# Kernel tuning notes

Hardware: AMD Instinct MI355X
Metric: run time of the kernel (lower is better)

## Reference

```python
import jax, jax.numpy as jnp
import numpy as np

N1 = 50000
N2 = 50000
E = 800000
D = 128
DOUT = 128
L = 2
NEG_SLOPE = 0.2


def setup_inputs() -> dict:
    key = jax.random.key(0)
    ks = jax.random.split(key, 32)
    s = 0.05
    inp = {
        "x1": jax.random.normal(ks[0], (N1, D), jnp.float32),
        "x2": jax.random.normal(ks[1], (N2, D), jnp.float32),
        "ei11": jax.random.randint(ks[2], (2, E), 0, N1, jnp.int32),
        "ei22": jax.random.randint(ks[3], (2, E), 0, N2, jnp.int32),
        "ei12": jnp.stack([
            jax.random.randint(ks[4], (E,), 0, N1, jnp.int32),
            jax.random.randint(ks[5], (E,), 0, N2, jnp.int32),
        ]),
        # intra protein_1 GATConv params (shared lin for src/dst), stacked over layers
        "W_i1": jax.random.normal(ks[6], (L, D, D), jnp.float32) * s,
        "as_i1": jax.random.normal(ks[7], (L, D), jnp.float32) * s,
        "ad_i1": jax.random.normal(ks[8], (L, D), jnp.float32) * s,
        "b_i1": jnp.zeros((L, D), jnp.float32),
        # intra protein_2
        "W_i2": jax.random.normal(ks[9], (L, D, D), jnp.float32) * s,
        "as_i2": jax.random.normal(ks[10], (L, D), jnp.float32) * s,
        "ad_i2": jax.random.normal(ks[11], (L, D), jnp.float32) * s,
        "b_i2": jnp.zeros((L, D), jnp.float32),
        # inter protein_1 -> protein_2 (bipartite: separate src/dst lin)
        "Ws_x": jax.random.normal(ks[12], (L, D, D), jnp.float32) * s,
        "Wd_x": jax.random.normal(ks[13], (L, D, D), jnp.float32) * s,
        "as_x": jax.random.normal(ks[14], (L, D), jnp.float32) * s,
        "ad_x": jax.random.normal(ks[15], (L, D), jnp.float32) * s,
        "b_x": jnp.zeros((L, D), jnp.float32),
        # final linear
        "W_out": jax.random.normal(ks[16], (D, DOUT), jnp.float32) * s,
        "b_out": jnp.zeros((DOUT,), jnp.float32),
    }
    return inp


def _segment_softmax(logits, seg, num_segments):
    m = jax.ops.segment_max(logits, seg, num_segments=num_segments)
    e = jnp.exp(logits - m[seg])
    z = jax.ops.segment_sum(e, seg, num_segments=num_segments)
    return e / (z[seg] + 1e-16)


def _gat(x_src, x_dst, ei, W_src, W_dst, a_s, a_d, b, num_dst):
    hs = x_src @ W_src                       # [Ns, D]
    hd = x_dst @ W_dst                       # [Nd, D]
    src, dst = ei[0], ei[1]
    logit = jax.nn.leaky_relu((hs @ a_s)[src] + (hd @ a_d)[dst], NEG_SLOPE)  # [E]
    coef = _segment_softmax(logit, dst, num_dst)  # [E]
    out = jax.ops.segment_sum(coef[:, None] * hs[src], dst, num_segments=num_dst)
    return out + b


def reference(x1, x2, ei11, ei22, ei12, W_i1, as_i1, ad_i1, b_i1,
              W_i2, as_i2, ad_i2, b_i2, Ws_x, Wd_x, as_x, ad_x, b_x,
              W_out, b_out):
    h1, h2 = x1, x2
    for l in range(L):
        o1 = _gat(h1, h1, ei11, W_i1[l], W_i1[l], as_i1[l], ad_i1[l], b_i1[l], N1)
        o2 = _gat(h2, h2, ei22, W_i2[l], W_i2[l], as_i2[l], ad_i2[l], b_i2[l], N2)
        o2 = o2 + _gat(h1, h2, ei12, Ws_x[l], Wd_x[l], as_x[l], ad_x[l], b_x[l], N2)
        h1 = jax.nn.relu(o1)
        h2 = jax.nn.relu(o2)
    return (h1 @ W_out + b_out, h2 @ W_out + b_out)
```

## Files before the change

### kernel.cpp

```cpp
#include <hip/hip_runtime.h>
#include <hip/hip_bf16.h>
#include <hip/hip_fp16.h>
#include <cstdint>

#define D 128
#define NEG 0.2f
#define WSH 8
#define WIN 256
#define CAP 5120

typedef _Float16 f16x8 __attribute__((ext_vector_type(8)));
typedef float f32x4 __attribute__((ext_vector_type(4)));

static __device__ __forceinline__ ushort f2h(float x) {
  __half h = __float2half(x);
  return *reinterpret_cast<ushort*>(&h);
}
static __device__ __forceinline__ float h2f(ushort u) {
  __half h = *reinterpret_cast<__half*>(&u);
  return __half2float(h);
}

__global__ __launch_bounds__(256) void bin3_kernel(
    const int* __restrict__ ei0, const int* __restrict__ ei1, const int* __restrict__ ei2,
    int E0, int E1, int E2,
    int* __restrict__ p0, int* __restrict__ p1, int* __restrict__ p2,
    int* __restrict__ bcnt) {
  int sset = blockIdx.y;
  const int* ei = sset == 0 ? ei0 : (sset == 1 ? ei1 : ei2);
  int E = sset == 0 ? E0 : (sset == 1 ? E1 : E2);
  int* pairs = sset == 0 ? p0 : (sset == 1 ? p1 : p2);
  int* bc = bcnt + sset * 256;
  const int* src = ei;
  const int* dst = ei + E;
  __shared__ int lcnt[WIN], lcur[WIN], lbase[WIN];
  int t = threadIdx.x;
  lcnt[t] = 0; lcur[t] = 0;
  __syncthreads();
  int base = blockIdx.x * 2048;
  int s[8], d[8];
  #pragma unroll
  for (int k = 0; k < 8; k++) {
    int e = base + k * 256 + t;
    if (e < E) {
      s[k] = src[e]; d[k] = dst[e];
      atomicAdd(&lcnt[d[k] >> WSH], 1);
    } else d[k] = -1;
  }
  __syncthreads();
  if (lcnt[t] > 0) lbase[t] = atomicAdd(&bc[t], lcnt[t]);
  __syncthreads();
  #pragma unroll
  for (int k = 0; k < 8; k++) {
    if (d[k] >= 0) {
      int b = d[k] >> WSH;
      int r = atomicAdd(&lcur[b], 1);
      int slot = lbase[b] + r;
      if (slot < CAP)
        pairs[(size_t)b * CAP + slot] = (s[k] & 0xFFFF) | ((d[k] & 255) << 16);
    }
  }
}

__global__ __launch_bounds__(256) void count3_kernel(
    const int* __restrict__ p0, const int* __restrict__ p1, const int* __restrict__ p2,
    const int* __restrict__ bcnt,
    int* __restrict__ cnt0, int* __restrict__ cnt1, int* __restrict__ cnt2,
    int* __restrict__ off0, int* __restrict__ off1, int* __restrict__ off2,
    int* __restrict__ wsum, int N0, int N1, int N2) {
  int sset = blockIdx.y;
  const int* pairs = sset == 0 ? p0 : (sset == 1 ? p1 : p2);
  int* cnt = sset == 0 ? cnt0 : (sset == 1 ? cnt1 : cnt2);
  int* offs = sset == 0 ? off0 : (sset == 1 ? off1 : off2);
  int N = sset == 0 ? N0 : (sset == 1 ? N1 : N2);
  const int* bc = bcnt + sset * 256;
  int* ws = wsum + sset * 256;
  __shared__ int h[WIN];
  __shared__ int sc[WIN];
  int b = blockIdx.x, t = threadIdx.x;
  h[t] = 0; __syncthreads();
  int n = bc[b]; if (n > CAP) n = CAP;
  const int* p = pairs + (size_t)b * CAP;
  for (int i = t; i < n; i += 256) atomicAdd(&h[(p[i] >> 16) & 255], 1);
  __syncthreads();
  int v = h[t]; sc[t] = v; __syncthreads();
  for (int o = 1; o < 256; o <<= 1) {
    int x = (t >= o) ? sc[t - o] : 0; __syncthreads();
    sc[t] += x; __syncthreads();
  }
  int node = b * WIN + t;
  if (node < N) { cnt[node] = v; offs[node] = sc[t] - v; }
  if (t == 255) ws[b] = sc[255];
}

__global__ void wscan3_kernel(int* wsum) {
  __shared__ int sc[256];
  int t = threadIdx.x;
  int* w = wsum + blockIdx.x * 256;
  int v = w[t];
  sc[t] = v; __syncthreads();
  for (int o = 1; o < 256; o <<= 1) {
    int x = (t >= o) ? sc[t - o] : 0; __syncthreads();
    sc[t] += x; __syncthreads();
  }
  w[t] = sc[t] - v;
}

__global__ __launch_bounds__(256) void fill23_kernel(
    const int* __restrict__ p0, const int* __restrict__ p1, const int* __restrict__ p2,
    const int* __restrict__ bcnt, const int* __restrict__ wsum,
    int* __restrict__ off0, int* __restrict__ off1, int* __restrict__ off2,
    ushort* __restrict__ cs0, ushort* __restrict__ cs1, ushort* __restrict__ cs2,
    int N0, int N1, int N2) {
  int sset = blockIdx.y;
  const int* pairs = sset == 0 ? p0 : (sset == 1 ? p1 : p2);
  int* offs = sset == 0 ? off0 : (sset == 1 ? off1 : off2);
  ushort* csrc = sset == 0 ? cs0 : (sset == 1 ? cs1 : cs2);
  int N = sset == 0 ? N0 : (sset == 1 ? N1 : N2);
  const int* bc = bcnt + sset * 256;
  __shared__ int cur[WIN];
  int b = blockIdx.x, t = threadIdx.x;
  int wb = wsum[sset * 256 + b];
  int node = b * WIN + t;
  int start = 0;
  if (node < N) { start = offs[node] + wb; offs[node] = start; }
  cur[t] = start;
  __syncthreads();
  int n = bc[b]; if (n > CAP) n = CAP;
  const int* p = pairs + (size_t)b * CAP;
  for (int i = t; i < n; i += 256) {
    int v = p[i];
    int pp = atomicAdd(&cur[(v >> 16) & 255], 1);
    csrc[pp] = (ushort)(v & 0xFFFF);
  }
}

__global__ __launch_bounds__(256) void wprep6_kernel(
    const float* __restrict__ W_i1, const float* __restrict__ W_i2,
    const float* __restrict__ Ws_x,
    ushort* __restrict__ WtA, ushort* __restrict__ WtB, ushort* __restrict__ WtX) {
  int b = blockIdx.x;
  int which = b >> 1, l = b & 1;
  const float* Wb = (which == 0 ? W_i1 : (which == 1 ? W_i2 : Ws_x)) + l * 16384;
  ushort* Wo = (which == 0 ? WtA : (which == 1 ? WtB : WtX)) + l * 16384;
  __shared__ float s[128 * 129];
  int t = threadIdx.x;
  #pragma unroll
  for (int i = 0; i < 16; i++) {
    int idx = i * 256 + t;
    int k = idx >> 5, n4 = idx & 31;
    float4 v = *(const float4*)&Wb[k * 128 + n4 * 4];
    s[k * 129 + n4 * 4 + 0] = v.x;
    s[k * 129 + n4 * 4 + 1] = v.y;
    s[k * 129 + n4 * 4 + 2] = v.z;
    s[k * 129 + n4 * 4 + 3] = v.w;
  }
  __syncthreads();
  #pragma unroll
  for (int i = 0; i < 8; i++) {
    int idx = i * 256 + t;
    int n = idx >> 4, k8 = (idx & 15) * 8;
    ushort4 h0, h1;
    h0.x = f2h(s[(k8 + 0) * 129 + n]); h0.y = f2h(s[(k8 + 1) * 129 + n]);
    h0.z = f2h(s[(k8 + 2) * 129 + n]); h0.w = f2h(s[(k8 + 3) * 129 + n]);
    h1.x = f2h(s[(k8 + 4) * 129 + n]); h1.y = f2h(s[(k8 + 5) * 129 + n]);
    h1.z = f2h(s[(k8 + 6) * 129 + n]); h1.w = f2h(s[(k8 + 7) * 129 + n]);
    *(ushort4*)&Wo[n * 128 + k8] = h0;
    *(ushort4*)&Wo[n * 128 + k8 + 4] = h1;
  }
}

__global__ __launch_bounds__(256) void wprepout_kernel(
    const float* __restrict__ W, ushort* __restrict__ Wh, ushort* __restrict__ Wl) {
  __shared__ float s[128 * 129];
  int t = threadIdx.x;
  #pragma unroll
  for (int i = 0; i < 16; i++) {
    int idx = i * 256 + t;
    int k = idx >> 5, n4 = idx & 31;
    float4 v = *(const float4*)&W[k * 128 + n4 * 4];
    s[k * 129 + n4 * 4 + 0] = v.x;
    s[k * 129 + n4 * 4 + 1] = v.y;
    s[k * 129 + n4 * 4 + 2] = v.z;
    s[k * 129 + n4 * 4 + 3] = v.w;
  }
  __syncthreads();
  #pragma unroll
  for (int i = 0; i < 8; i++) {
    int idx = i * 256 + t;
    int n = idx >> 4, k8 = (idx & 15) * 8;
    ushort hh[8], ll[8];
    #pragma unroll
    for (int e = 0; e < 8; e++) {
      float w = s[(k8 + e) * 129 + n];
      hh[e] = f2h(w);
      ll[e] = f2h(w - h2f(hh[e]));
    }
    *(ushort4*)&Wh[n * 128 + k8]     = make_ushort4(hh[0], hh[1], hh[2], hh[3]);
    *(ushort4*)&Wh[n * 128 + k8 + 4] = make_ushort4(hh[4], hh[5], hh[6], hh[7]);
    *(ushort4*)&Wl[n * 128 + k8]     = make_ushort4(ll[0], ll[1], ll[2], ll[3]);
    *(ushort4*)&Wl[n * 128 + k8 + 4] = make_ushort4(ll[4], ll[5], ll[6], ll[7]);
  }
}

__global__ void wvec2_kernel(const float* __restrict__ Wd, const float* __restrict__ ad,
                             float* __restrict__ wv) {
  int l = blockIdx.x;
  int r = threadIdx.x;
  const float* Wb = Wd + (size_t)l * 16384;
  const float* ab = ad + l * 128;
  float s = 0.f;
  for (int c = 0; c < D; c++) s += Wb[r * D + c] * ab[c];
  wv[l * 128 + r] = s;
}

#define SWZ(b) ((b) ^ ((((b) >> 8) & 7) << 4))

template <int XF16>
__global__ __launch_bounds__(256) void gemm16_kernel(
    const void* __restrict__ Xv, const ushort* __restrict__ Wt,
    ushort* __restrict__ Yb,
    const float* __restrict__ a_sv, const float* __restrict__ a_dv,
    const float* __restrict__ wvec,
    float* __restrict__ aSo, float* __restrict__ aDo, float* __restrict__ aXo, int M) {
  __shared__ ushort sX[64 * 128];
  __shared__ ushort sW[128 * 128];
  __shared__ float sv[128];
  int t = threadIdx.x;
  int bm = blockIdx.x * 64;
  {
    const uint4* W4 = (const uint4*)Wt;
    #pragma unroll
    for (int i = 0; i < 8; i++) {
      int idx = i * 256 + t;
      int byte = idx * 16;
      *(uint4*)((char*)sW + SWZ(byte)) = W4[idx];
    }
  }
  {
    #pragma unroll
    for (int i = 0; i < 8; i++) {
      int idx = i * 256 + t;
      int row = idx >> 5, c4 = idx & 31;
      ushort4 h = make_ushort4(0, 0, 0, 0);
      if (bm + row < M) {
        if (XF16) {
          h = *(const ushort4*)((const ushort*)Xv + (size_t)(bm + row) * 128 + c4 * 4);
        } else {
          float4 v = ((const float4*)Xv)[(size_t)(bm + row) * 32 + c4];
          h.x = f2h(v.x); h.y = f2h(v.y); h.z = f2h(v.z); h.w = f2h(v.w);
        }
      }
      int byte = idx * 8;
      *(uint2*)((char*)sX + SWZ(byte)) = *(uint2*)&h;
    }
  }
  if (wvec != nullptr && t < 128) sv[t] = wvec[t];
  __syncthreads();

  int w = t >> 6, l = t & 63;
  int lq = l >> 4, lr = l & 15;
  int xrow = w * 16 + lr;
  f32x4 acc[8] = {};
  float ax = 0.f;
  #pragma unroll
  for (int kk = 0; kk < 4; kk++) {
    int xb = xrow * 256 + kk * 64 + lq * 16;
    f16x8 xa = *(const f16x8*)((const char*)sX + SWZ(xb));
    if (wvec != nullptr) {
      float4 w0 = *(const float4*)&sv[kk * 32 + lq * 8];
      float4 w1 = *(const float4*)&sv[kk * 32 + lq * 8 + 4];
      ax += (float)xa[0] * w0.x + (float)xa[1] * w0.y + (float)xa[2] * w0.z + (float)xa[3] * w0.w
          + (float)xa[4] * w1.x + (float)xa[5] * w1.y + (float)xa[6] * w1.z + (float)xa[7] * w1.w;
    }
    #pragma unroll
    for (int ct = 0; ct < 8; ct++) {
      int nb = (ct * 16 + lr) * 256 + kk * 64 + lq * 16;
      f16x8 wa = *(const f16x8*)((const char*)sW + SWZ(nb));
      acc[ct] = __builtin_amdgcn_mfma_f32_16x16x32_f16(wa, xa, acc[ct], 0, 0, 0);
    }
  }
  int row_m = bm + xrow;
  bool valid = row_m < M;
  #pragma unroll
  for (int ct = 0; ct < 8; ct++) {
    ushort4 h;
    h.x = f2h(acc[ct][0]); h.y = f2h(acc[ct][1]);
    h.z = f2h(acc[ct][2]); h.w = f2h(acc[ct][3]);
    if (valid) *(ushort4*)&Yb[(size_t)row_m * 128 + ct * 16 + lq * 4] = h;
  }
  if (a_sv != nullptr) {
    float s = 0.f;
    #pragma unroll
    for (int ct = 0; ct < 8; ct++) {
      float4 a = *(const float4*)&a_sv[ct * 16 + lq * 4];
      s += acc[ct][0] * a.x + acc[ct][1] * a.y + acc[ct][2] * a.z + acc[ct][3] * a.w;
    }
    s += __shfl_xor(s, 16); s += __shfl_xor(s, 32);
    if (valid && lq == 0) aSo[row_m] = s;
  }
  if (a_dv != nullptr) {
    float s = 0.f;
    #pragma unroll
    for (int ct = 0; ct < 8; ct++) {
      float4 a = *(const float4*)&a_dv[ct * 16 + lq * 4];
      s += acc[ct][0] * a.x + acc[ct][1] * a.y + acc[ct][2] * a.z + acc[ct][3] * a.w;
    }
    s += __shfl_xor(s, 16); s += __shfl_xor(s, 32);
    if (valid && lq == 0) aDo[row_m] = s;
  }
  if (wvec != nullptr) {
    ax += __shfl_xor(ax, 16); ax += __shfl_xor(ax, 32);
    if (valid && lq == 0) aXo[row_m] = ax;
  }
}

template <int XF16>
__global__ __launch_bounds__(256) void gemmx2_kernel(
    const void* __restrict__ Xv,
    const ushort* __restrict__ Wt0, const ushort* __restrict__ Wt1,
    ushort* __restrict__ Yb0, ushort* __restrict__ Yb1,
    const float* __restrict__ asv0, const float* __restrict__ asv1,
    const float* __restrict__ adv1,
    float* __restrict__ aSo0, float* __restrict__ aSo1, float* __restrict__ aDo1,
    int M) {
  int y = blockIdx.y;
  const ushort* Wt = y ? Wt1 : Wt0;
  ushort* Yb = y ? Yb1 : Yb0;
  const float* a_sv = y ? asv1 : asv0;
  const float* a_dv = y ? adv1 : nullptr;
  float* aSo = y ? aSo1 : aSo0;
  float* aDo = aDo1;
  __shared__ ushort sX[64 * 128];
  __shared__ ushort sW[128 * 128];
  int t = threadIdx.x;
  int bm = blockIdx.x * 64;
  {
    const uint4* W4 = (const uint4*)Wt;
    #pragma unroll
    for (int i = 0; i < 8; i++) {
      int idx = i * 256 + t;
      int byte = idx * 16;
      *(uint4*)((char*)sW + SWZ(byte)) = W4[idx];
    }
  }
  {
    #pragma unroll
    for (int i = 0; i < 8; i++) {
      int idx = i * 256 + t;
      int row = idx >> 5, c4 = idx & 31;
      ushort4 h = make_ushort4(0, 0, 0, 0);
      if (bm + row < M) {
        if (XF16) {
          h = *(const ushort4*)((const ushort*)Xv + (size_t)(bm + row) * 128 + c4 * 4);
        } else {
          float4 v = ((const float4*)Xv)[(size_t)(bm + row) * 32 + c4];
          h.x = f2h(v.x); h.y = f2h(v.y); h.z = f2h(v.z); h.w = f2h(v.w);
        }
      }
      int byte = idx * 8;
      *(uint2*)((char*)sX + SWZ(byte)) = *(uint2*)&h;
    }
  }
  __syncthreads();
  int w = t >> 6, l = t & 63;
  int lq = l >> 4, lr = l & 15;
  int xrow = w * 16 + lr;
  f32x4 acc[8] = {};
  #pragma unroll
  for (int kk = 0; kk < 4; kk++) {
    int xb = xrow * 256 + kk * 64 + lq * 16;
    f16x8 xa = *(const f16x8*)((const char*)sX + SWZ(xb));
    #pragma unroll
    for (int ct = 0; ct < 8; ct++) {
      int nb = (ct * 16 + lr) * 256 + kk * 64 + lq * 16;
      f16x8 wa = *(const f16x8*)((const char*)sW + SWZ(nb));
      acc[ct] = __builtin_amdgcn_mfma_f32_16x16x32_f16(wa, xa, acc[ct], 0, 0, 0);
    }
  }
  int row_m = bm + xrow;
  bool valid = row_m < M;
  #pragma unroll
  for (int ct = 0; ct < 8; ct++) {
    ushort4 h;
    h.x = f2h(acc[ct][0]); h.y = f2h(acc[ct][1]);
    h.z = f2h(acc[ct][2]); h.w = f2h(acc[ct][3]);
    if (valid) *(ushort4*)&Yb[(size_t)row_m * 128 + ct * 16 + lq * 4] = h;
  }
  {
    float s = 0.f;
    #pragma unroll
    for (int ct = 0; ct < 8; ct++) {
      float4 a = *(const float4*)&a_sv[ct * 16 + lq * 4];
      s += acc[ct][0] * a.x + acc[ct][1] * a.y + acc[ct][2] * a.z + acc[ct][3] * a.w;
    }
    s += __shfl_xor(s, 16); s += __shfl_xor(s, 32);
    if (valid && lq == 0) aSo[row_m] = s;
  }
  if (a_dv != nullptr) {
    float s = 0.f;
    #pragma unroll
    for (int ct = 0; ct < 8; ct++) {
      float4 a = *(const float4*)&a_dv[ct * 16 + lq * 4];
      s += acc[ct][0] * a.x + acc[ct][1] * a.y + acc[ct][2] * a.z + acc[ct][3] * a.w;
    }
    s += __shfl_xor(s, 16); s += __shfl_xor(s, 32);
    if (valid && lq == 0) aDo[row_m] = s;
  }
}

__global__ __launch_bounds__(512) void gemmfin_kernel(
    const ushort* __restrict__ XA, const ushort* __restrict__ XB,
    const ushort* __restrict__ Wh, const ushort* __restrict__ Wl,
    const float* __restrict__ bias,
    float* __restrict__ YA, float* __restrict__ YB, int MA, int MB, int mgA) {
  int bid = blockIdx.x;
  const ushort* X; float* Y; int M, bm;
  if (bid < mgA) { X = XA; Y = YA; M = MA; bm = bid * 128; }
  else           { X = XB; Y = YB; M = MB; bm = (bid - mgA) * 128; }
  __shared__ ushort sWh[128 * 128];
  __shared__ ushort sWl[128 * 128];
  __shared__ ushort sH[128 * 128];
  int t = threadIdx.x;
  {
    const uint4* Wh4 = (const uint4*)Wh;
    const uint4* Wl4 = (const uint4*)Wl;
    #pragma unroll
    for (int i = 0; i < 4; i++) {
      int idx = i * 512 + t;
      int byte = idx * 16;
      *(uint4*)((char*)sWh + SWZ(byte)) = Wh4[idx];
      *(uint4*)((char*)sWl + SWZ(byte)) = Wl4[idx];
    }
  }
  {
    const uint4* X4 = (const uint4*)X;
    #pragma unroll
    for (int i = 0; i < 4; i++) {
      int idx = i * 512 + t;
      int row = idx >> 4, c8 = idx & 15;
      uint4 v = make_uint4(0, 0, 0, 0);
      if (bm + row < M) v = X4[(size_t)(bm + row) * 16 + c8];
      *(uint4*)((char*)sH + SWZ(idx * 16)) = v;
    }
  }
  __syncthreads();
  int w = t >> 6, l = t & 63;
  int lq = l >> 4, lr = l & 15;
  int xrow = w * 16 + lr;
  f32x4 acc[8] = {};
  #pragma unroll
  for (int kk = 0; kk < 4; kk++) {
    int xb = xrow * 256 + kk * 64 + lq * 16;
    f16x8 xh = *(const f16x8*)((const char*)sH + SWZ(xb));
    #pragma unroll
    for (int ct = 0; ct < 8; ct++) {
      int nb = (ct * 16 + lr) * 256 + kk * 64 + lq * 16;
      f16x8 wh = *(const f16x8*)((const char*)sWh + SWZ(nb));
      f16x8 wl = *(const f16x8*)((const char*)sWl + SWZ(nb));
      acc[ct] = __builtin_amdgcn_mfma_f32_16x16x32_f16(wh, xh, acc[ct], 0, 0, 0);
      acc[ct] = __builtin_amdgcn_mfma_f32_16x16x32_f16(wl, xh, acc[ct], 0, 0, 0);
    }
  }
  int row_m = bm + xrow;
  if (row_m < M) {
    #pragma unroll
    for (int ct = 0; ct < 8; ct++) {
      float4 b = *(const float4*)&bias[ct * 16 + lq * 4];
      float4 o = make_float4(acc[ct][0] + b.x, acc[ct][1] + b.y,
                             acc[ct][2] + b.z, acc[ct][3] + b.w);
      *(float4*)&Y[(size_t)row_m * 128 + ct * 16 + lq * 4] = o;
    }
  }
}

static __device__ __forceinline__ void gather_rows(
    const ushort* __restrict__ hs, const float* __restrict__ aSv, float adv,
    int st, int deg, const ushort* __restrict__ cs,
    int lane, int quarter, int q, float acc[8], float& z) {
  for (int base = 0; base < deg; base += 64) {
    int m = deg - base; if (m > 64) m = 64;
    int sidx = 0; float el = 0.f;
    if (lane < m) {
      sidx = cs[st + base + lane];
      float l = aSv[sidx] + adv;
      l = (l > 0.f) ? l : NEG * l;
      el = __expf(l);
    }
    float zs = el;
    for (int o = 32; o > 0; o >>= 1) zs += __shfl_xor(zs, o);
    z += zs;
    #pragma unroll 4
    for (int j = 0; j < m; j += 4) {
      int jj = j + quarter;
      int sj = __shfl(sidx, jj);
      float ej = __shfl(el, jj);
      uint4 hv = *(const uint4*)(hs + (size_t)sj * D + q * 8);
      float2 f0 = __half22float2(*reinterpret_cast<__half2*>(&hv.x));
      float2 f1 = __half22float2(*reinterpret_cast<__half2*>(&hv.y));
      float2 f2 = __half22float2(*reinterpret_cast<__half2*>(&hv.z));
      float2 f3 = __half22float2(*reinterpret_cast<__half2*>(&hv.w));
      acc[0] += ej * f0.x; acc[1] += ej * f0.y;
      acc[2] += ej * f1.x; acc[3] += ej * f1.y;
      acc[4] += ej * f2.x; acc[5] += ej * f2.y;
      acc[6] += ej * f3.x; acc[7] += ej * f3.y;
    }
  }
}

__global__ __launch_bounds__(256) void agg1_kernel(
    const ushort* __restrict__ hs, const float* __restrict__ aS, const float* __restrict__ aD,
    const int* __restrict__ offs, const int* __restrict__ cnt, const ushort* __restrict__ csrc,
    const float* __restrict__ bias1, ushort* __restrict__ out, int N) {
  int wid = threadIdx.x >> 6, lane = threadIdx.x & 63;
  int d = blockIdx.x * 4 + wid;
  if (d >= N) return;
  int quarter = lane >> 4, q = lane & 15;
  float acc[8] = {}; float z = 0.f;
  gather_rows(hs, aS, aD[d], offs[d], cnt[d], csrc, lane, quarter, q, acc, z);
  float inv = 1.f / (z + 1e-16f);
  float res[8];
  #pragma unroll
  for (int k = 0; k < 8; k++) res[k] = acc[k] * inv;
  #pragma unroll
  for (int k = 0; k < 8; k++) {
    res[k] += __shfl_xor(res[k], 16);
    res[k] += __shfl_xor(res[k], 32);
  }
  if (quarter == 0) {
    float4 b0 = *(const float4*)(bias1 + q * 8);
    float4 b1 = *(const float4*)(bias1 + q * 8 + 4);
    res[0]+=b0.x; res[1]+=b0.y; res[2]+=b0.z; res[3]+=b0.w;
    res[4]+=b1.x; res[5]+=b1.y; res[6]+=b1.z; res[7]+=b1.w;
    #pragma unroll
    for (int k = 0; k < 8; k++) res[k] = res[k] > 0.f ? res[k] : 0.f;
    size_t rb = (size_t)d * D + q * 8;
    *(ushort4*)(out + rb)     = make_ushort4(f2h(res[0]), f2h(res[1]), f2h(res[2]), f2h(res[3]));
    *(ushort4*)(out + rb + 4) = make_ushort4(f2h(res[4]), f2h(res[5]), f2h(res[6]), f2h(res[7]));
  }
}

__global__ __launch_bounds__(256) void agg2_kernel(
    const ushort* __restrict__ hs1, const float* __restrict__ aS1, const float* __restrict__ aD1,
    const int* __restrict__ off1, const int* __restrict__ cnt1, const ushort* __restrict__ cs1,
    const ushort* __restrict__ hs2, const float* __restrict__ aS2v, const float* __restrict__ aD2v,
    const int* __restrict__ off2, const int* __restrict__ cnt2, const ushort* __restrict__ cs2,
    const float* __restrict__ bias1, const float* __restrict__ bias2,
    ushort* __restrict__ out, int N) {
  int wid = threadIdx.x >> 6, lane = threadIdx.x & 63;
  int d = blockIdx.x * 4 + wid;
  if (d >= N) return;
  int quarter = lane >> 4, q = lane & 15;
  float acc1[8] = {}; float z1 = 0.f;
  gather_rows(hs1, aS1, aD1[d], off1[d], cnt1[d], cs1, lane, quarter, q, acc1, z1);
  float acc2[8] = {}; float z2 = 0.f;
  gather_rows(hs2, aS2v, aD2v[d], off2[d], cnt2[d], cs2, lane, quarter, q, acc2, z2);
  float inv1 = 1.f / (z1 + 1e-16f);
  float inv2 = 1.f / (z2 + 1e-16f);
  float res[8];
  #pragma unroll
  for (int k = 0; k < 8; k++) res[k] = acc1[k] * inv1 + acc2[k] * inv2;
  #pragma unroll
  for (int k = 0; k < 8; k++) {
    res[k] += __shfl_xor(res[k], 16);
    res[k] += __shfl_xor(res[k], 32);
  }
  if (quarter == 0) {
    float4 b0 = *(const float4*)(bias1 + q * 8);
    float4 b1 = *(const float4*)(bias1 + q * 8 + 4);
    float4 c0 = *(const float4*)(bias2 + q * 8);
    float4 c1 = *(const float4*)(bias2 + q * 8 + 4);
    res[0]+=b0.x+c0.x; res[1]+=b0.y+c0.y; res[2]+=b0.z+c0.z; res[3]+=b0.w+c0.w;
    res[4]+=b1.x+c1.x; res[5]+=b1.y+c1.y; res[6]+=b1.z+c1.z; res[7]+=b1.w+c1.w;
    #pragma unroll
    for (int k = 0; k < 8; k++) res[k] = res[k] > 0.f ? res[k] : 0.f;
    size_t rb = (size_t)d * D + q * 8;
    *(ushort4*)(out + rb)     = make_ushort4(f2h(res[0]), f2h(res[1]), f2h(res[2]), f2h(res[3]));
    *(ushort4*)(out + rb + 4) = make_ushort4(f2h(res[4]), f2h(res[5]), f2h(res[6]), f2h(res[7]));
  }
}

extern "C" void kernel_launch(void* const* d_in, const int* in_sizes, int n_in,
                              void* d_out, int out_size, void* d_ws, size_t ws_size,
                              hipStream_t stream) {
  const float* x1   = (const float*)d_in[0];
  const float* x2   = (const float*)d_in[1];
  const int*   ei11 = (const int*)d_in[2];
  const int*   ei22 = (const int*)d_in[3];
  const int*   ei12 = (const int*)d_in[4];
  const float* W_i1 = (const float*)d_in[5];
  const float* as_i1= (const float*)d_in[6];
  const float* ad_i1= (const float*)d_in[7];
  const float* b_i1 = (const float*)d_in[8];
  const float* W_i2 = (const float*)d_in[9];
  const float* as_i2= (const float*)d_in[10];
  const float* ad_i2= (const float*)d_in[11];
  const float* b_i2 = (const float*)d_in[12];
  const float* Ws_x = (const float*)d_in[13];
  const float* Wd_x = (const float*)d_in[14];
  const float* as_x = (const float*)d_in[15];
  const float* ad_x = (const float*)d_in[16];
  const float* b_x  = (const float*)d_in[17];
  const float* W_out= (const float*)d_in[18];
  const float* b_out= (const float*)d_in[19];

  int N1 = in_sizes[0] / D, N2 = in_sizes[1] / D;
  int E11 = in_sizes[2] / 2, E22 = in_sizes[3] / 2, E12 = in_sizes[4] / 2;
  int Nmax = (N1 > N2) ? N1 : N2;
  int Emax = E11 > E22 ? (E11 > E12 ? E11 : E12) : (E22 > E12 ? E22 : E12);
  int NB1 = (N1 + WIN - 1) / WIN, NB2 = (N2 + WIN - 1) / WIN;
  int NBmax = (NB1 > NB2) ? NB1 : NB2;

  float* outA = (float*)d_out;
  float* outB = outA + (size_t)N1 * D;

  char* w = (char*)d_ws;
  auto alloc = [&](size_t b) { char* p = w; w += (b + 255) & ~(size_t)255; return p; };
  size_t pair_bytes = (size_t)NBmax * CAP * 4;
  size_t hsmax = (size_t)Nmax * D * 2;
  ushort* BB  = (ushort*)alloc(hsmax > pair_bytes ? hsmax : pair_bytes);
  ushort* BX  = (ushort*)alloc(hsmax > pair_bytes ? hsmax : pair_bytes);
  ushort* h1  = (ushort*)alloc(((size_t)N1 * D * 2) > pair_bytes ? ((size_t)N1 * D * 2) : pair_bytes);
  ushort* h2  = (ushort*)alloc((size_t)N2 * D * 2);
  int* pairs0 = (int*)BB;
  int* pairs1 = (int*)BX;
  int* pairs2 = (int*)h1;
  float* aS   = (float*)alloc((size_t)Nmax * 4);
  float* aD   = (float*)alloc((size_t)Nmax * 4);
  float* aDx  = (float*)alloc((size_t)Nmax * 4);
  float* aS2  = (float*)alloc((size_t)Nmax * 4);
  float* wvecB= (float*)alloc(256 * 4);
  ushort* WtA = (ushort*)alloc(2 * 16384 * 2);
  ushort* WtB = (ushort*)alloc(2 * 16384 * 2);
  ushort* WtX = (ushort*)alloc(2 * 16384 * 2);
  ushort* Wfh = (ushort*)alloc(16384 * 2);
  ushort* Wfl = (ushort*)alloc(16384 * 2);
  int* bcnt  = (int*)alloc(3 * 256 * 4);
  int* wsum  = (int*)alloc(3 * 256 * 4);
  int* cnt11 = (int*)alloc((size_t)N1 * 4);
  int* off11 = (int*)alloc((size_t)N1 * 4);
  ushort* csA = (ushort*)alloc((size_t)E11 * 2);
  int* cnt22 = (int*)alloc((size_t)N2 * 4);
  int* off22 = (int*)alloc((size_t)N2 * 4);
  ushort* csB = (ushort*)alloc((size_t)E22 * 2);
  int* cnt12 = (int*)alloc((size_t)N2 * 4);
  int* off12 = (int*)alloc((size_t)N2 * 4);
  ushort* csC = (ushort*)alloc((size_t)E12 * 2);

  hipMemsetAsync(bcnt, 0, 3 * 256 * 4, stream);
  bin3_kernel<<<dim3((Emax + 2047) / 2048, 3), 256, 0, stream>>>(
      ei11, ei22, ei12, E11, E22, E12, pairs0, pairs1, pairs2, bcnt);
  count3_kernel<<<dim3(NBmax, 3), 256, 0, stream>>>(
      pairs0, pairs1, pairs2, bcnt, cnt11, cnt22, cnt12,
      off11, off22, off12, wsum, N1, N2, N2);
  wscan3_kernel<<<3, 256, 0, stream>>>(wsum);
  fill23_kernel<<<dim3(NBmax, 3), 256, 0, stream>>>(
      pairs0, pairs1, pairs2, bcnt, wsum, off11, off22, off12,
      csA, csB, csC, N1, N2, N2);

  wprep6_kernel<<<6, 256, 0, stream>>>(W_i1, W_i2, Ws_x, WtA, WtB, WtX);
  wprepout_kernel<<<1, 256, 0, stream>>>(W_out, Wfh, Wfl);
  wvec2_kernel<<<2, 128, 0, stream>>>(Wd_x, ad_x, wvecB);

  int mg1 = (N1 + 63) / 64, mg2 = (N2 + 63) / 64;
  int fg1 = (N1 + 127) / 128, fg2 = (N2 + 127) / 128;
  int gg1 = (N1 + 3) / 4, gg2 = (N2 + 3) / 4;
  ushort* hsA = BB;
  ushort* hsB = BB;
  ushort* hsX = BX;

  gemmx2_kernel<0><<<dim3(mg1, 2), 256, 0, stream>>>(x1, WtX, WtA, hsX, hsA,
      as_x, as_i1, ad_i1, aS2, aS, aD, N1);
  agg1_kernel<<<gg1, 256, 0, stream>>>(hsA, aS, aD, off11, cnt11, csA, b_i1, h1, N1);
  gemm16_kernel<0><<<mg2, 256, 0, stream>>>(x2, WtB, hsB,
      as_i2, ad_i2, wvecB, aS, aD, aDx, N2);
  agg2_kernel<<<gg2, 256, 0, stream>>>(hsB, aS, aD, off22, cnt22, csB,
      hsX, aS2, aDx, off12, cnt12, csC, b_i2, b_x, h2, N2);

  gemmx2_kernel<1><<<dim3(mg1, 2), 256, 0, stream>>>(h1, WtX + 16384, WtA + 16384,
      hsX, hsA, as_x + 128, as_i1 + 128, ad_i1 + 128, aS2, aS, aD, N1);
  agg1_kernel<<<gg1, 256, 0, stream>>>(hsA, aS, aD, off11, cnt11, csA,
      b_i1 + 128, h1, N1);
  gemm16_kernel<1><<<mg2, 256, 0, stream>>>(h2, WtB + 16384, hsB,
      as_i2 + 128, ad_i2 + 128, wvecB + 128, aS, aD, aDx, N2);
  agg2_kernel<<<gg2, 256, 0, stream>>>(hsB, aS, aD, off22, cnt22, csB,
      hsX, aS2, aDx, off12, cnt12, csC, b_i2 + 128, b_x + 128, h2, N2);

  gemmfin_kernel<<<fg1 + fg2, 512, 0, stream>>>(h1, h2, Wfh, Wfl, b_out,
                                                outA, outB, N1, N2, fg1);
}
```

Before: 384.0 us.

## Fuse CSR build, weight prep, and per-layer GEMMs into fewer launches

Merges the count, window-scan and fill stages of CSR construction into one kernel, with each block redoing the small 256-entry prefix scan over bin counts. Folds the three weight-prep kernels into one launch. Fuses the three per-layer projection GEMMs (inter, intra-1, intra-2) into a single 3-way grid by giving each GEMM its own output buffers, removing launch overhead and a serialization point. Also unrolls the gather loop by four so independent row loads are in flight together, at the cost of extra buffers and registers.

```diff
diff --git a/kernel.cpp b/kernel.cpp
--- a/kernel.cpp
+++ b/kernel.cpp
@@ -62,89 +62,78 @@
   }
 }
 
-__global__ __launch_bounds__(256) void count3_kernel(
+__global__ __launch_bounds__(256) void countfill3_kernel(
     const int* __restrict__ p0, const int* __restrict__ p1, const int* __restrict__ p2,
     const int* __restrict__ bcnt,
     int* __restrict__ cnt0, int* __restrict__ cnt1, int* __restrict__ cnt2,
-    int* __restrict__ off0, int* __restrict__ off1, int* __restrict__ off2,
-    int* __restrict__ wsum, int N0, int N1, int N2) {
-  int sset = blockIdx.y;
-  const int* pairs = sset == 0 ? p0 : (sset == 1 ? p1 : p2);
-  int* cnt = sset == 0 ? cnt0 : (sset == 1 ? cnt1 : cnt2);
-  int* offs = sset == 0 ? off0 : (sset == 1 ? off1 : off2);
-  int N = sset == 0 ? N0 : (sset == 1 ? N1 : N2);
-  const int* bc = bcnt + sset * 256;
-  int* ws = wsum + sset * 256;
-  __shared__ int h[WIN];
-  __shared__ int sc[WIN];
-  int b = blockIdx.x, t = threadIdx.x;
-  h[t] = 0; __syncthreads();
-  int n = bc[b]; if (n > CAP) n = CAP;
-  const int* p = pairs + (size_t)b * CAP;
-  for (int i = t; i < n; i += 256) atomicAdd(&h[(p[i] >> 16) & 255], 1);
-  __syncthreads();
-  int v = h[t]; sc[t] = v; __syncthreads();
-  for (int o = 1; o < 256; o <<= 1) {
-    int x = (t >= o) ? sc[t - o] : 0; __syncthreads();
-    sc[t] += x; __syncthreads();
-  }
-  int node = b * WIN + t;
-  if (node < N) { cnt[node] = v; offs[node] = sc[t] - v; }
-  if (t == 255) ws[b] = sc[255];
-}
-
-__global__ void wscan3_kernel(int* wsum) {
-  __shared__ int sc[256];
-  int t = threadIdx.x;
-  int* w = wsum + blockIdx.x * 256;
-  int v = w[t];
-  sc[t] = v; __syncthreads();
-  for (int o = 1; o < 256; o <<= 1) {
-    int x = (t >= o) ? sc[t - o] : 0; __syncthreads();
-    sc[t] += x; __syncthreads();
-  }
-  w[t] = sc[t] - v;
-}
-
-__global__ __launch_bounds__(256) void fill23_kernel(
-    const int* __restrict__ p0, const int* __restrict__ p1, const int* __restrict__ p2,
-    const int* __restrict__ bcnt, const int* __restrict__ wsum,
     int* __restrict__ off0, int* __restrict__ off1, int* __restrict__ off2,
     ushort* __restrict__ cs0, ushort* __restrict__ cs1, ushort* __restrict__ cs2,
     int N0, int N1, int N2) {
   int sset = blockIdx.y;
   const int* pairs = sset == 0 ? p0 : (sset == 1 ? p1 : p2);
+  int* cnt = sset == 0 ? cnt0 : (sset == 1 ? cnt1 : cnt2);
   int* offs = sset == 0 ? off0 : (sset == 1 ? off1 : off2);
   ushort* csrc = sset == 0 ? cs0 : (sset == 1 ? cs1 : cs2);
   int N = sset == 0 ? N0 : (sset == 1 ? N1 : N2);
   const int* bc = bcnt + sset * 256;
-  __shared__ int cur[WIN];
+  __shared__ int h[WIN], sc[WIN], wbs[WIN], cur[WIN];
   int b = blockIdx.x, t = threadIdx.x;
-  int wb = wsum[sset * 256 + b];
+  int bcv = bc[t]; if (bcv > CAP) bcv = CAP;
+  wbs[t] = bcv;
+  h[t] = 0;
+  __syncthreads();
+  for (int o = 1; o < 256; o <<= 1) {
+    int x = (t >= o) ? wbs[t - o] : 0; __syncthreads();
+    wbs[t] += x; __syncthreads();
+  }
+  int n = bc[b]; if (n > CAP) n = CAP;
+  int wb = wbs[b] - n;
+  const int* p = pairs + (size_t)b * CAP;
+  for (int i = t; i < n; i += 256) atomicAdd(&h[(p[i] >> 16) & 255], 1);
+  __syncthreads();
+  int v = h[t]; sc[t] = v;
+  __syncthreads();
+  for (int o = 1; o < 256; o <<= 1) {
+    int x = (t >= o) ? sc[t - o] : 0; __syncthreads();
+    sc[t] += x; __syncthreads();
+  }
+  int start = sc[t] - v + wb;
   int node = b * WIN + t;
-  int start = 0;
-  if (node < N) { start = offs[node] + wb; offs[node] = start; }
+  if (node < N) { cnt[node] = v; offs[node] = start; }
   cur[t] = start;
   __syncthreads();
-  int n = bc[b]; if (n > CAP) n = CAP;
-  const int* p = pairs + (size_t)b * CAP;
   for (int i = t; i < n; i += 256) {
-    int v = p[i];
-    int pp = atomicAdd(&cur[(v >> 16) & 255], 1);
-    csrc[pp] = (ushort)(v & 0xFFFF);
-  }
-}
-
-__global__ __launch_bounds__(256) void wprep6_kernel(
+    int pv = p[i];
+    int pp = atomicAdd(&cur[(pv >> 16) & 255], 1);
+    csrc[pp] = (ushort)(pv & 0xFFFF);
+  }
+}
+
+__global__ __launch_bounds__(256) void prep_kernel(
     const float* __restrict__ W_i1, const float* __restrict__ W_i2,
-    const float* __restrict__ Ws_x,
-    ushort* __restrict__ WtA, ushort* __restrict__ WtB, ushort* __restrict__ WtX) {
+    const float* __restrict__ Ws_x, const float* __restrict__ W_out,
+    const float* __restrict__ Wd_x, const float* __restrict__ ad_x,
+    ushort* __restrict__ WtA, ushort* __restrict__ WtB, ushort* __restrict__ WtX,
+    ushort* __restrict__ Wfh, ushort* __restrict__ Wfl, float* __restrict__ wv) {
   int b = blockIdx.x;
-  int which = b >> 1, l = b & 1;
-  const float* Wb = (which == 0 ? W_i1 : (which == 1 ? W_i2 : Ws_x)) + l * 16384;
-  ushort* Wo = (which == 0 ? WtA : (which == 1 ? WtB : WtX)) + l * 16384;
+  int t = threadIdx.x;
+  if (b >= 7) {
+    int l = b - 7;
+    if (t < 128) {
+      const float* Wb = Wd_x + (size_t)l * 16384;
+      const float* ab = ad_x + l * 128;
+      float s = 0.f;
+      for (int c = 0; c < D; c++) s += Wb[t * D + c] * ab[c];
+      wv[l * 128 + t] = s;
+    }
+    return;
+  }
   __shared__ float s[128 * 129];
-  int t = threadIdx.x;
+  const float* Wb;
+  if (b < 6) {
+    int which = b >> 1, l = b & 1;
+    Wb = (which == 0 ? W_i1 : (which == 1 ? W_i2 : Ws_x)) + l * 16384;
+  } else Wb = W_out;
   #pragma unroll
   for (int i = 0; i < 16; i++) {
     int idx = i * 256 + t;
@@ -156,85 +145,77 @@
     s[k * 129 + n4 * 4 + 3] = v.w;
   }
   __syncthreads();
-  #pragma unroll
-  for (int i = 0; i < 8; i++) {
-    int idx = i * 256 + t;
-    int n = idx >> 4, k8 = (idx & 15) * 8;
-    ushort4 h0, h1;
-    h0.x = f2h(s[(k8 + 0) * 129 + n]); h0.y = f2h(s[(k8 + 1) * 129 + n]);
-    h0.z = f2h(s[(k8 + 2) * 129 + n]); h0.w = f2h(s[(k8 + 3) * 129 + n]);
-    h1.x = f2h(s[(k8 + 4) * 129 + n]); h1.y = f2h(s[(k8 + 5) * 129 + n]);
-    h1.z = f2h(s[(k8 + 6) * 129 + n]); h1.w = f2h(s[(k8 + 7) * 129 + n]);
-    *(ushort4*)&Wo[n * 128 + k8] = h0;
-    *(ushort4*)&Wo[n * 128 + k8 + 4] = h1;
-  }
-}
-
-__global__ __launch_bounds__(256) void wprepout_kernel(
-    const float* __restrict__ W, ushort* __restrict__ Wh, ushort* __restrict__ Wl) {
-  __shared__ float s[128 * 129];
-  int t = threadIdx.x;
-  #pragma unroll
-  for (int i = 0; i < 16; i++) {
-    int idx = i * 256 + t;
-    int k = idx >> 5, n4 = idx & 31;
-    float4 v = *(const float4*)&W[k * 128 + n4 * 4];
-    s[k * 129 + n4 * 4 + 0] = v.x;
-    s[k * 129 + n4 * 4 + 1] = v.y;
-    s[k * 129 + n4 * 4 + 2] = v.z;
-    s[k * 129 + n4 * 4 + 3] = v.w;
-  }
-  __syncthreads();
-  #pragma unroll
-  for (int i = 0; i < 8; i++) {
-    int idx = i * 256 + t;
-    int n = idx >> 4, k8 = (idx & 15) * 8;
-    ushort hh[8], ll[8];
-    #pragma unroll
-    for (int e = 0; e < 8; e++) {
-      float w = s[(k8 + e) * 129 + n];
-      hh[e] = f2h(w);
-      ll[e] = f2h(w - h2f(hh[e]));
-    }
-    *(ushort4*)&Wh[n * 128 + k8]     = make_ushort4(hh[0], hh[1], hh[2], hh[3]);
-    *(ushort4*)&Wh[n * 128 + k8 + 4] = make_ushort4(hh[4], hh[5], hh[6], hh[7]);
-    *(ushort4*)&Wl[n * 128 + k8]     = make_ushort4(ll[0], ll[1], ll[2], ll[3]);
-    *(ushort4*)&Wl[n * 128 + k8 + 4] = make_ushort4(ll[4], ll[5], ll[6], ll[7]);
-  }
-}
-
-__global__ void wvec2_kernel(const float* __restrict__ Wd, const float* __restrict__ ad,
-                             float* __restrict__ wv) {
-  int l = blockIdx.x;
-  int r = threadIdx.x;
-  const float* Wb = Wd + (size_t)l * 16384;
-  const float* ab = ad + l * 128;
-  float s = 0.f;
-  for (int c = 0; c < D; c++) s += Wb[r * D + c] * ab[c];
-  wv[l * 128 + r] = s;
+  if (b < 6) {
+    int which = b >> 1, l = b & 1;
+    ushort* Wo = (which == 0 ? WtA : (which == 1 ? WtB : WtX)) + l * 16384;
+    #pragma unroll
+    for (int i = 0; i < 8; i++) {
+      int idx = i * 256 + t;
+      int n = idx >> 4, k8 = (idx & 15) * 8;
+      ushort4 h0, h1;
+      h0.x = f2h(s[(k8 + 0) * 129 + n]); h0.y = f2h(s[(k8 + 1) * 129 + n]);
+      h0.z = f2h(s[(k8 + 2) * 129 + n]); h0.w = f2h(s[(k8 + 3) * 129 + n]);
+      h1.x = f2h(s[(k8 + 4) * 129 + n]); h1.y = f2h(s[(k8 + 5) * 129 + n]);
+      h1.z = f2h(s[(k8 + 6) * 129 + n]); h1.w = f2h(s[(k8 + 7) * 129 + n]);
+      *(ushort4*)&Wo[n * 128 + k8] = h0;
+      *(ushort4*)&Wo[n * 128 + k8 + 4] = h1;
+    }
+  } else {
+    #pragma unroll
+    for (int i = 0; i < 8; i++) {
+      int idx = i * 256 + t;
+      int n = idx >> 4, k8 = (idx & 15) * 8;
+      ushort hh[8], ll[8];
+      #pragma unroll
+      for (int e = 0; e < 8; e++) {
+        float w = s[(k8 + e) * 129 + n];
+        hh[e] = f2h(w);
+        ll[e] = f2h(w - h2f(hh[e]));
+      }
+      *(ushort4*)&Wfh[n * 128 + k8]     = make_ushort4(hh[0], hh[1], hh[2], hh[3]);
+      *(ushort4*)&Wfh[n * 128 + k8 + 4] = make_ushort4(hh[4], hh[5], hh[6], hh[7]);
+      *(ushort4*)&Wfl[n * 128 + k8]     = make_ushort4(ll[0], ll[1], ll[2], ll[3]);
+      *(ushort4*)&Wfl[n * 128 + k8 + 4] = make_ushort4(ll[4], ll[5], ll[6], ll[7]);
+    }
+  }
 }
 
 #define SWZ(b) ((b) ^ ((((b) >> 8) & 7) << 4))
 
 template <int XF16>
-__global__ __launch_bounds__(256) void gemm16_kernel(
-    const void* __restrict__ Xv, const ushort* __restrict__ Wt,
-    ushort* __restrict__ Yb,
-    const float* __restrict__ a_sv, const float* __restrict__ a_dv,
-    const float* __restrict__ wvec,
-    float* __restrict__ aSo, float* __restrict__ aDo, float* __restrict__ aXo, int M) {
+__global__ __launch_bounds__(256) void gemmx3_kernel(
+    const void* __restrict__ Xv1, const void* __restrict__ Xv2,
+    const ushort* __restrict__ WtX_, const ushort* __restrict__ WtA_,
+    const ushort* __restrict__ WtB_,
+    ushort* __restrict__ YbX, ushort* __restrict__ YbA, ushort* __restrict__ YbB,
+    const float* __restrict__ asx, const float* __restrict__ as1,
+    const float* __restrict__ ad1, const float* __restrict__ as2,
+    const float* __restrict__ ad2, const float* __restrict__ wvec,
+    float* __restrict__ aSxo, float* __restrict__ aS1o, float* __restrict__ aD1o,
+    float* __restrict__ aS2o, float* __restrict__ aD2o, float* __restrict__ aXo,
+    int M1, int M2) {
+  int y = blockIdx.y;
+  const void* Xv = (y == 2) ? Xv2 : Xv1;
+  int M = (y == 2) ? M2 : M1;
+  int bm = blockIdx.x * 64;
+  if (bm >= M) return;
+  const ushort* Wt = y == 0 ? WtX_ : (y == 1 ? WtA_ : WtB_);
+  ushort* Yb = y == 0 ? YbX : (y == 1 ? YbA : YbB);
+  const float* a_sv = y == 0 ? asx : (y == 1 ? as1 : as2);
+  const float* a_dv = y == 0 ? nullptr : (y == 1 ? ad1 : ad2);
+  const float* wv = (y == 2) ? wvec : nullptr;
+  float* aSo = y == 0 ? aSxo : (y == 1 ? aS1o : aS2o);
+  float* aDo = (y == 1) ? aD1o : aD2o;
   __shared__ ushort sX[64 * 128];
   __shared__ ushort sW[128 * 128];
   __shared__ float sv[128];
   int t = threadIdx.x;
-  int bm = blockIdx.x * 64;
   {
     const uint4* W4 = (const uint4*)Wt;
     #pragma unroll
     for (int i = 0; i < 8; i++) {
       int idx = i * 256 + t;
-      int byte = idx * 16;
-      *(uint4*)((char*)sW + SWZ(byte)) = W4[idx];
+      *(uint4*)((char*)sW + SWZ(idx * 16)) = W4[idx];
     }
   }
   {
@@ -251,11 +232,10 @@
           h.x = f2h(v.x); h.y = f2h(v.y); h.z = f2h(v.z); h.w = f2h(v.w);
         }
       }
-      int byte = idx * 8;
-      *(uint2*)((char*)sX + SWZ(byte)) = *(uint2*)&h;
-    }
-  }
-  if (wvec != nullptr && t < 128) sv[t] = wvec[t];
+      *(uint2*)((char*)sX + SWZ(idx * 8)) = *(uint2*)&h;
+    }
+  }
+  if (wv != nullptr && t < 128) sv[t] = wv[t];
   __syncthreads();
 
   int w = t >> 6, l = t & 63;
@@ -267,7 +247,7 @@
   for (int kk = 0; kk < 4; kk++) {
     int xb = xrow * 256 + kk * 64 + lq * 16;
     f16x8 xa = *(const f16x8*)((const char*)sX + SWZ(xb));
-    if (wvec != nullptr) {
+    if (wv != nullptr) {
       float4 w0 = *(const float4*)&sv[kk * 32 + lq * 8];
       float4 w1 = *(const float4*)&sv[kk * 32 + lq * 8 + 4];
       ax += (float)xa[0] * w0.x + (float)xa[1] * w0.y + (float)xa[2] * w0.z + (float)xa[3] * w0.w
@@ -289,7 +269,7 @@
     h.z = f2h(acc[ct][2]); h.w = f2h(acc[ct][3]);
     if (valid) *(ushort4*)&Yb[(size_t)row_m * 128 + ct * 16 + lq * 4] = h;
   }
-  if (a_sv != nullptr) {
+  {
     float s = 0.f;
     #pragma unroll
     for (int ct = 0; ct < 8; ct++) {
@@ -309,103 +289,9 @@
     s += __shfl_xor(s, 16); s += __shfl_xor(s, 32);
     if (valid && lq == 0) aDo[row_m] = s;
   }
-  if (wvec != nullptr) {
+  if (wv != nullptr) {
     ax += __shfl_xor(ax, 16); ax += __shfl_xor(ax, 32);
     if (valid && lq == 0) aXo[row_m] = ax;
-  }
-}
-
-template <int XF16>
-__global__ __launch_bounds__(256) void gemmx2_kernel(
-    const void* __restrict__ Xv,
-    const ushort* __restrict__ Wt0, const ushort* __restrict__ Wt1,
-    ushort* __restrict__ Yb0, ushort* __restrict__ Yb1,
-    const float* __restrict__ asv0, const float* __restrict__ asv1,
-    const float* __restrict__ adv1,
-    float* __restrict__ aSo0, float* __restrict__ aSo1, float* __restrict__ aDo1,
-    int M) {
-  int y = blockIdx.y;
-  const ushort* Wt = y ? Wt1 : Wt0;
-  ushort* Yb = y ? Yb1 : Yb0;
-  const float* a_sv = y ? asv1 : asv0;
-  const float* a_dv = y ? adv1 : nullptr;
-  float* aSo = y ? aSo1 : aSo0;
-  float* aDo = aDo1;
-  __shared__ ushort sX[64 * 128];
-  __shared__ ushort sW[128 * 128];
-  int t = threadIdx.x;
-  int bm = blockIdx.x * 64;
-  {
-    const uint4* W4 = (const uint4*)Wt;
-    #pragma unroll
-    for (int i = 0; i < 8; i++) {
-      int idx = i * 256 + t;
-      int byte = idx * 16;
-      *(uint4*)((char*)sW + SWZ(byte)) = W4[idx];
-    }
-  }
-  {
-    #pragma unroll
-    for (int i = 0; i < 8; i++) {
-      int idx = i * 256 + t;
-      int row = idx >> 5, c4 = idx & 31;
-      ushort4 h = make_ushort4(0, 0, 0, 0);
-      if (bm + row < M) {
-        if (XF16) {
-          h = *(const ushort4*)((const ushort*)Xv + (size_t)(bm + row) * 128 + c4 * 4);
-        } else {
-          float4 v = ((const float4*)Xv)[(size_t)(bm + row) * 32 + c4];
-          h.x = f2h(v.x); h.y = f2h(v.y); h.z = f2h(v.z); h.w = f2h(v.w);
-        }
-      }
-      int byte = idx * 8;
-      *(uint2*)((char*)sX + SWZ(byte)) = *(uint2*)&h;
-    }
-  }
-  __syncthreads();
-  int w = t >> 6, l = t & 63;
-  int lq = l >> 4, lr = l & 15;
-  int xrow = w * 16 + lr;
-  f32x4 acc[8] = {};
-  #pragma unroll
-  for (int kk = 0; kk < 4; kk++) {
-    int xb = xrow * 256 + kk * 64 + lq * 16;
-    f16x8 xa = *(const f16x8*)((const char*)sX + SWZ(xb));
-    #pragma unroll
-    for (int ct = 0; ct < 8; ct++) {
-      int nb = (ct * 16 + lr) * 256 + kk * 64 + lq * 16;
-      f16x8 wa = *(const f16x8*)((const char*)sW + SWZ(nb));
-      acc[ct] = __builtin_amdgcn_mfma_f32_16x16x32_f16(wa, xa, acc[ct], 0, 0, 0);
-    }
-  }
-  int row_m = bm + xrow;
-  bool valid = row_m < M;
-  #pragma unroll
-  for (int ct = 0; ct < 8; ct++) {
-    ushort4 h;
-    h.x = f2h(acc[ct][0]); h.y = f2h(acc[ct][1]);
-    h.z = f2h(acc[ct][2]); h.w = f2h(acc[ct][3]);
-    if (valid) *(ushort4*)&Yb[(size_t)row_m * 128 + ct * 16 + lq * 4] = h;
-  }
-  {
-    float s = 0.f;
-    #pragma unroll
-    for (int ct = 0; ct < 8; ct++) {
-      float4 a = *(const float4*)&a_sv[ct * 16 + lq * 4];
-      s += acc[ct][0] * a.x + acc[ct][1] * a.y + acc[ct][2] * a.z + acc[ct][3] * a.w;
-    }
-    s += __shfl_xor(s, 16); s += __shfl_xor(s, 32);
-    if (valid && lq == 0) aSo[row_m] = s;
-  }
-  if (a_dv != nullptr) {
-    float s = 0.f;
-    #pragma unroll
-    for (int ct = 0; ct < 8; ct++) {
-      float4 a = *(const float4*)&a_dv[ct * 16 + lq * 4];
-      s += acc[ct][0] * a.x + acc[ct][1] * a.y + acc[ct][2] * a.z + acc[ct][3] * a.w;
-    }
-    s += __shfl_xor(s, 16); s += __shfl_xor(s, 32);
-    if (valid && lq == 0) aDo[row_m] = s;
   }
 }
 
@@ -428,9 +314,8 @@
     #pragma unroll
     for (int i = 0; i < 4; i++) {
       int idx = i * 512 + t;
-      int byte = idx * 16;
-      *(uint4*)((char*)sWh + SWZ(byte)) = Wh4[idx];
-      *(uint4*)((char*)sWl + SWZ(byte)) = Wl4[idx];
+      *(uint4*)((char*)sWh + SWZ(idx * 16)) = Wh4[idx];
+      *(uint4*)((char*)sWl + SWZ(idx * 16)) = Wl4[idx];
     }
   }
   {
@@ -473,6 +358,16 @@
     }
   }
 }
+
+#define ACC8(hv, ej) { \
+  float2 f0 = __half22float2(*reinterpret_cast<__half2*>(&hv.x)); \
+  float2 f1 = __half22float2(*reinterpret_cast<__half2*>(&hv.y)); \
+  float2 f2 = __half22float2(*reinterpret_cast<__half2*>(&hv.z)); \
+  float2 f3 = __half22float2(*reinterpret_cast<__half2*>(&hv.w)); \
+  acc[0] += ej * f0.x; acc[1] += ej * f0.y; \
+  acc[2] += ej * f1.x; acc[3] += ej * f1.y; \
+  acc[4] += ej * f2.x; acc[5] += ej * f2.y; \
+  acc[6] += ej * f3.x; acc[7] += ej * f3.y; }
 
 static __device__ __forceinline__ void gather_rows(
     const ushort* __restrict__ hs, const float* __restrict__ aSv, float adv,
@@ -490,20 +385,20 @@
     float zs = el;
     for (int o = 32; o > 0; o >>= 1) zs += __shfl_xor(zs, o);
     z += zs;
-    #pragma unroll 4
-    for (int j = 0; j < m; j += 4) {
-      int jj = j + quarter;
-      int sj = __shfl(sidx, jj);
-      float ej = __shfl(el, jj);
-      uint4 hv = *(const uint4*)(hs + (size_t)sj * D + q * 8);
-      float2 f0 = __half22float2(*reinterpret_cast<__half2*>(&hv.x));
-      float2 f1 = __half22float2(*reinterpret_cast<__half2*>(&hv.y));
-      float2 f2 = __half22float2(*reinterpret_cast<__half2*>(&hv.z));
-      float2 f3 = __half22float2(*reinterpret_cast<__half2*>(&hv.w));
-      acc[0] += ej * f0.x; acc[1] += ej * f0.y;
-      acc[2] += ej * f1.x; acc[3] += ej * f1.y;
-      acc[4] += ej * f2.x; acc[5] += ej * f2.y;
-      acc[6] += ej * f3.x; acc[7] += ej * f3.y;
+    for (int j = 0; j < m; j += 16) {
+      int s0 = __shfl(sidx, j + quarter);
+      int s1 = __shfl(sidx, j + 4 + quarter);
+      int s2 = __shfl(sidx, j + 8 + quarter);
+      int s3 = __shfl(sidx, j + 12 + quarter);
+      float e0 = __shfl(el, j + quarter);
+      float e1 = __shfl(el, j + 4 + quarter);
+      float e2 = __shfl(el, j + 8 + quarter);
+      float e3 = __shfl(el, j + 12 + quarter);
+      uint4 h0 = *(const uint4*)(hs + (size_t)s0 * D + q * 8);
+      uint4 h1 = *(const uint4*)(hs + (size_t)s1 * D + q * 8);
+      uint4 h2 = *(const uint4*)(hs + (size_t)s2 * D + q * 8);
+      uint4 h3 = *(const uint4*)(hs + (size_t)s3 * D + q * 8);
+      ACC8(h0, e0); ACC8(h1, e1); ACC8(h2, e2); ACC8(h3, e3);
     }
   }
 }
@@ -552,9 +447,15 @@
   if (d >= N) return;
   int quarter = lane >> 4, q = lane & 15;
   float acc1[8] = {}; float z1 = 0.f;
-  gather_rows(hs1, aS1, aD1[d], off1[d], cnt1[d], cs1, lane, quarter, q, acc1, z1);
+  {
+    float* acc = acc1;
+    gather_rows(hs1, aS1, aD1[d], off1[d], cnt1[d], cs1, lane, quarter, q, acc, z1);
+  }
   float acc2[8] = {}; float z2 = 0.f;
-  gather_rows(hs2, aS2v, aD2v[d], off2[d], cnt2[d], cs2, lane, quarter, q, acc2, z2);
+  {
+    float* acc = acc2;
+    gather_rows(hs2, aS2v, aD2v[d], off2[d], cnt2[d], cs2, lane, quarter, q, acc, z2);
+  }
   float inv1 = 1.f / (z1 + 1e-16f);
   float inv2 = 1.f / (z2 + 1e-16f);
   float res[8];
@@ -618,17 +519,21 @@
   auto alloc = [&](size_t b) { char* p = w; w += (b + 255) & ~(size_t)255; return p; };
   size_t pair_bytes = (size_t)NBmax * CAP * 4;
   size_t hsmax = (size_t)Nmax * D * 2;
-  ushort* BB  = (ushort*)alloc(hsmax > pair_bytes ? hsmax : pair_bytes);
-  ushort* BX  = (ushort*)alloc(hsmax > pair_bytes ? hsmax : pair_bytes);
-  ushort* h1  = (ushort*)alloc(((size_t)N1 * D * 2) > pair_bytes ? ((size_t)N1 * D * 2) : pair_bytes);
+  size_t big = hsmax > pair_bytes ? hsmax : pair_bytes;
+  ushort* BA  = (ushort*)alloc(big);
+  ushort* BX  = (ushort*)alloc(big);
+  ushort* h1  = (ushort*)alloc(big);
+  ushort* BB2 = (ushort*)alloc(hsmax);
   ushort* h2  = (ushort*)alloc((size_t)N2 * D * 2);
-  int* pairs0 = (int*)BB;
+  int* pairs0 = (int*)BA;
   int* pairs1 = (int*)BX;
   int* pairs2 = (int*)h1;
-  float* aS   = (float*)alloc((size_t)Nmax * 4);
-  float* aD   = (float*)alloc((size_t)Nmax * 4);
+  float* aSx  = (float*)alloc((size_t)Nmax * 4);
+  float* aS1  = (float*)alloc((size_t)Nmax * 4);
+  float* aD1  = (float*)alloc((size_t)Nmax * 4);
+  float* aS2b = (float*)alloc((size_t)Nmax * 4);
+  float* aD2b = (float*)alloc((size_t)Nmax * 4);
   float* aDx  = (float*)alloc((size_t)Nmax * 4);
-  float* aS2  = (float*)alloc((size_t)Nmax * 4);
   float* wvecB= (float*)alloc(256 * 4);
   ushort* WtA = (ushort*)alloc(2 * 16384 * 2);
   ushort* WtB = (ushort*)alloc(2 * 16384 * 2);
@@ -636,7 +541,6 @@
   ushort* Wfh = (ushort*)alloc(16384 * 2);
   ushort* Wfl = (ushort*)alloc(16384 * 2);
   int* bcnt  = (int*)alloc(3 * 256 * 4);
-  int* wsum  = (int*)alloc(3 * 256 * 4);
   int* cnt11 = (int*)alloc((size_t)N1 * 4);
   int* off11 = (int*)alloc((size_t)N1 * 4);
   ushort* csA = (ushort*)alloc((size_t)E11 * 2);
@@ -650,41 +554,37 @@
   hipMemsetAsync(bcnt, 0, 3 * 256 * 4, stream);
   bin3_kernel<<<dim3((Emax + 2047) / 2048, 3), 256, 0, stream>>>(
       ei11, ei22, ei12, E11, E22, E12, pairs0, pairs1, pairs2, bcnt);
-  count3_kernel<<<dim3(NBmax, 3), 256, 0, stream>>>(
+  countfill3_kernel<<<dim3(NBmax, 3), 256, 0, stream>>>(
       pairs0, pairs1, pairs2, bcnt, cnt11, cnt22, cnt12,
-      off11, off22, off12, wsum, N1, N2, N2);
-  wscan3_kernel<<<3, 256, 0, stream>>>(wsum);
-  fill23_kernel<<<dim3(NBmax, 3), 256, 0, stream>>>(
-      pairs0, pairs1, pairs2, bcnt, wsum, off11, off22, off12,
-      csA, csB, csC, N1, N2, N2);
-
-  wprep6_kernel<<<6, 256, 0, stream>>>(W_i1, W_i2, Ws_x, WtA, WtB, WtX);
-  wprepout_kernel<<<1, 256, 0, stream>>>(W_out, Wfh, Wfl);
-  wvec2_kernel<<<2, 128, 0, stream>>>(Wd_x, ad_x, wvecB);
+      off11, off22, off12, csA, csB, csC, N1, N2, N2);
+
+  prep_kernel<<<9, 256, 0, stream>>>(W_i1, W_i2, Ws_x, W_out, Wd_x, ad_x,
+                                     WtA, WtB, WtX, Wfh, Wfl, wvecB);
 
   int mg1 = (N1 + 63) / 64, mg2 = (N2 + 63) / 64;
+  int mgmax = mg1 > mg2 ? mg1 : mg2;
   int fg1 = (N1 + 127) / 128, fg2 = (N2 + 127) / 128;
   int gg1 = (N1 + 3) / 4, gg2 = (N2 + 3) / 4;
-  ushort* hsA = BB;
-  ushort* hsB = BB;
+  ushort* hsA = BA;
   ushort* hsX = BX;
-
-  gemmx2_kernel<0><<<dim3(mg1, 2), 256, 0, stream>>>(x1, WtX, WtA, hsX, hsA,
-      as_x, as_i1, ad_i1, aS2, aS, aD, N1);
-  agg1_kernel<<<gg1, 256, 0, stream>>>(hsA, aS, aD, off11, cnt11, csA, b_i1, h1, N1);
-  gemm16_kernel<0><<<mg2, 256, 0, stream>>>(x2, WtB, hsB,
-      as_i2, ad_i2, wvecB, aS, aD, aDx, N2);
-  agg2_kernel<<<gg2, 256, 0, stream>>>(hsB, aS, aD, off22, cnt22, csB,
-      hsX, aS2, aDx, off12, cnt12, csC, b_i2, b_x, h2, N2);
-
-  gemmx2_kernel<1><<<dim3(mg1, 2), 256, 0, stream>>>(h1, WtX + 16384, WtA + 16384,
-      hsX, hsA, as_x + 128, as_i1 + 128, ad_i1 + 128, aS2, aS, aD, N1);
-  agg1_kernel<<<gg1, 256, 0, stream>>>(hsA, aS, aD, off11, cnt11, csA,
+  ushort* hsB = BB2;
+
+  gemmx3_kernel<0><<<dim3(mgmax, 3), 256, 0, stream>>>(
+      x1, x2, WtX, WtA, WtB, hsX, hsA, hsB,
+      as_x, as_i1, ad_i1, as_i2, ad_i2, wvecB,
+      aSx, aS1, aD1, aS2b, aD2b, aDx, N1, N2);
+  agg1_kernel<<<gg1, 256, 0, stream>>>(hsA, aS1, aD1, off11, cnt11, csA, b_i1, h1, N1);
+  agg2_kernel<<<gg2, 256, 0, stream>>>(hsB, aS2b, aD2b, off22, cnt22, csB,
+      hsX, aSx, aDx, off12, cnt12, csC, b_i2, b_x, h2, N2);
+
+  gemmx3_kernel<1><<<dim3(mgmax, 3), 256, 0, stream>>>(
+      h1, h2, WtX + 16384, WtA + 16384, WtB + 16384, hsX, hsA, hsB,
+      as_x + 128, as_i1 + 128, ad_i1 + 128, as_i2 + 128, ad_i2 + 128, wvecB + 128,
+      aSx, aS1, aD1, aS2b, aD2b, aDx, N1, N2);
+  agg1_kernel<<<gg1, 256, 0, stream>>>(hsA, aS1, aD1, off11, cnt11, csA,
       b_i1 + 128, h1, N1);
-  gemm16_kernel<1><<<mg2, 256, 0, stream>>>(h2, WtB + 16384, hsB,
-      as_i2 + 128, ad_i2 + 128, wvecB + 128, aS, aD, aDx, N2);
-  agg2_kernel<<<gg2, 256, 0, stream>>>(hsB, aS, aD, off22, cnt22, csB,
-      hsX, aS2, aDx, off12, cnt12, csC, b_i2 + 128, b_x + 128, h2, N2);
+  agg2_kernel<<<gg2, 256, 0, stream>>>(hsB, aS2b, aD2b, off22, cnt22, csB,
+      hsX, aSx, aDx, off12, cnt12, csC, b_i2 + 128, b_x + 128, h2, N2);
 
   gemmfin_kernel<<<fg1 + fg2, 512, 0, stream>>>(h1, h2, Wfh, Wfl, b_out,
                                                 outA, outB, N1, N2, fg1);
```

Result: faster. 361.6 us (-5.8%).
